# Performance work log

Measured on AMD Instinct MI355X. Metric: run time of the kernel, lower is better.

## Reference

```python
import jax, jax.numpy as jnp
import numpy as np

EPS = 1e-6

def setup_inputs() -> dict:
    key = jax.random.key(0)
    ks = jax.random.split(key, 8)
    I, S, O = 1024, 512, 1024
    Bsz, T = 4, 2048
    return {
        "u": jax.random.normal(ks[0], (Bsz, T, I), dtype=jnp.float32),
        "dt": jax.random.normal(ks[1], (S,), dtype=jnp.float32),
        "A": jax.random.normal(ks[2], (S,), dtype=jnp.float32),
        "Bmat": jax.random.normal(ks[3], (I, S), dtype=jnp.float32) / np.sqrt(S),
        "C": jax.random.normal(ks[4], (S, O), dtype=jnp.float32) / np.sqrt(S),
        "D": jax.random.normal(ks[5], (O,), dtype=jnp.float32),
        "norm_w": jnp.ones((I,), dtype=jnp.float32),
    }

def _rmsnorm(x, w):
    x32 = x.astype(jnp.float32)
    n = x32 * jax.lax.rsqrt(jnp.mean(x32 * x32, axis=-1, keepdims=True) + EPS)
    return n.astype(x.dtype) * w

def reference(u, dt, A, Bmat, C, D, norm_w):
    u = _rmsnorm(u, norm_w)                      # [B, T, I]
    Bsz, T, _ = u.shape
    dts = jax.nn.sigmoid(dt)                     # [S]
    a = jnp.exp(-dts * jnp.abs(A))               # [S] discretized decay
    t = jnp.arange(T, dtype=jnp.float32)
    h = dts[:, None] * a[:, None] ** t[None, :]  # [S, T] geometric kernel
    u_proj = jnp.einsum('bti,is->bst', u, Bmat)  # [B, S, T]
    # depthwise causal conv: flipped kernel + cross-correlation == convolution
    k = jnp.flip(h, axis=1)[:, None, :]          # [S, 1, T] (OIW)
    x = jax.lax.conv_general_dilated(
        u_proj, k, window_strides=(1,), padding=[(T - 1, T - 1)],
        dimension_numbers=('NCW', 'OIW', 'NCW'),
        feature_group_count=u_proj.shape[1])[:, :, :T]  # [B, S, T]
    x = jnp.transpose(x, (0, 2, 1))              # [B, T, S]
    y = jnp.einsum('bts,so->bto', x, C) + D      # [B, T, O]
    return (y, x[:, -1])
```

## Files before the change

kernel.cpp:

```cpp
#include <hip/hip_runtime.h>
#include <math.h>

#define I_DIM 1024
#define S_DIM 512
#define O_DIM 1024
#define T_DIM 2048
#define B_SZ 4
#define M_ROWS (B_SZ * T_DIM)
#define EPSF 1e-6f

#define CL 64
#define NCH 32

typedef _Float16 f16;
typedef __attribute__((ext_vector_type(8))) _Float16 f16x8;
typedef __attribute__((ext_vector_type(2))) _Float16 f16x2;
typedef __attribute__((ext_vector_type(4))) float f32x4;

__device__ __forceinline__ unsigned short f2h_bits(float f) {
    _Float16 h = (_Float16)f;
    return __builtin_bit_cast(unsigned short, h);
}

__device__ __forceinline__ void load16_lds(const void* g, void* l) {
    __builtin_amdgcn_global_load_lds((const __attribute__((address_space(1))) void*)g,
                                     (__attribute__((address_space(3))) void*)l,
                                     16, 0, 0);
}

__global__ __launch_bounds__(256)
void prep_w(const float* __restrict__ Bmat, const float* __restrict__ dt,
            const float* __restrict__ nw, unsigned short* __restrict__ Bt16,
            const float* __restrict__ Cmat, unsigned short* __restrict__ Ct16) {
    __shared__ float tile[32][33];
    const int t = threadIdx.x;
    const int tx = t & 31, ty = t >> 5;
    const int bx = blockIdx.x;
    if (bx < 512) {
        const int bs = (bx & 15) * 32;
        const int bi = (bx >> 4) * 32;
        #pragma unroll
        for (int i = ty; i < 32; i += 8)
            tile[i][tx] = Bmat[(size_t)(bi + i) * S_DIM + bs + tx];
        __syncthreads();
        const float w = nw[bi + tx];
        #pragma unroll
        for (int i = ty; i < 32; i += 8) {
            const int s = bs + i;
            const float dts = 1.0f / (1.0f + expf(-dt[s]));
            Bt16[(size_t)s * I_DIM + bi + tx] = f2h_bits(tile[tx][i] * dts * w);
        }
    } else {
        const int tb = bx - 512;
        const int bo = (tb & 31) * 32;
        const int bs = (tb >> 5) * 32;
        #pragma unroll
        for (int i = ty; i < 32; i += 8)
            tile[i][tx] = Cmat[(size_t)(bs + i) * O_DIM + bo + tx];
        __syncthreads();
        #pragma unroll
        for (int i = ty; i < 32; i += 8)
            Ct16[(size_t)(bo + i) * S_DIM + bs + tx] = f2h_bits(tile[tx][i]);
    }
}

__global__ __launch_bounds__(256)
void gemm1_rms_chfin(const float* __restrict__ U, const f16* __restrict__ Bt,
                     f16* __restrict__ up, float* __restrict__ chlast,
                     const float* __restrict__ dt, const float* __restrict__ Avec) {
    constexpr int K = I_DIM, N = S_DIM, LDA = 80, NK = K / 32;
    __shared__ __align__(16) unsigned char AsB[2][64 * LDA];
    __shared__ f16 Bs[2][128 * 32];
    __shared__ float rsbuf[64];
    const int t = threadIdx.x;

    int bid = blockIdx.x;
    bid = (bid & 7) * 64 + (bid >> 3);
    const int n0 = (bid & 3) * 128;
    const int m0 = (bid >> 2) * 64;
    const int wid = t >> 6, lane = t & 63;
    const int wn = wid * 32, lr = lane & 15, kg = lane >> 4;

    const float* aptr = U + (size_t)(m0 + (t >> 2)) * K + (t & 3) * 8;
    const f16*  bptr = Bt + (size_t)(n0 + (t >> 2)) * K + (t & 3) * 8;
    unsigned char* adst0 = &AsB[0][(t >> 2) * LDA + (t & 3) * 16];
    unsigned char* adst1 = &AsB[1][(t >> 2) * LDA + (t & 3) * 16];

    float ss = 0.f;
    f32x4 acc[4][2];
    #pragma unroll
    for (int i = 0; i < 4; ++i)
        #pragma unroll
        for (int j = 0; j < 2; ++j) acc[i][j] = (f32x4){0.f, 0.f, 0.f, 0.f};

    float4 ra, rb;
    auto cvt_write = [&](unsigned char* dst) {
        ss += ra.x * ra.x + ra.y * ra.y + ra.z * ra.z + ra.w * ra.w
            + rb.x * rb.x + rb.y * rb.y + rb.z * rb.z + rb.w * rb.w;
        f16x8 h = { (_Float16)ra.x, (_Float16)ra.y, (_Float16)ra.z, (_Float16)ra.w,
                    (_Float16)rb.x, (_Float16)rb.y, (_Float16)rb.z, (_Float16)rb.w };
        *(f16x8*)dst = h;
    };

    load16_lds(bptr, &Bs[0][t * 8]);
    load16_lds(bptr + (size_t)64 * K, &Bs[0][2048 + t * 8]);
    ra = *(const float4*)(aptr);
    rb = *(const float4*)(aptr + 4);
    cvt_write(adst0);
    __syncthreads();

    for (int kt = 0; kt < NK; ++kt) {
        const int cur = kt & 1;
        if (kt + 1 < NK) {
            const int k1 = (kt + 1) * 32;
            load16_lds(bptr + k1, &Bs[cur ^ 1][t * 8]);
            load16_lds(bptr + (size_t)64 * K + k1, &Bs[cur ^ 1][2048 + t * 8]);
            ra = *(const float4*)(aptr + k1);
            rb = *(const float4*)(aptr + k1 + 4);
        }
        f16x8 af[4], bf[2];
        #pragma unroll
        for (int m = 0; m < 4; ++m)
            af[m] = *(const f16x8*)&AsB[cur][(m * 16 + lr) * LDA + kg * 16];
        #pragma unroll
        for (int n = 0; n < 2; ++n)
            bf[n] = *(const f16x8*)&Bs[cur][(wn + n * 16 + lr) * 32 + kg * 8];
        #pragma unroll
        for (int m = 0; m < 4; ++m)
            #pragma unroll
            for (int n = 0; n < 2; ++n)
                acc[m][n] = __builtin_amdgcn_mfma_f32_16x16x32_f16(af[m], bf[n], acc[m][n], 0, 0, 0);
        if (kt + 1 < NK) cvt_write(cur == 0 ? adst1 : adst0);
        __syncthreads();
    }

    ss += __shfl_xor(ss, 1, 64);
    ss += __shfl_xor(ss, 2, 64);
    if ((t & 3) == 0) rsbuf[t >> 2] = rsqrtf(ss * (1.0f / K) + EPSF);
    __syncthreads();

    const int cb = m0 >> 11;
    const int cc = (m0 >> 6) & (NCH - 1);
    #pragma unroll
    for (int n = 0; n < 2; ++n) {
        const int col = n0 + wn + n * 16 + lr;
        const float dts = 1.0f / (1.0f + expf(-dt[col]));
        const float e = dts * fabsf(Avec[col]);
        const float ainv = expf(e);
        float partial = 0.f;
        #pragma unroll
        for (int m = 0; m < 4; ++m) {
            const int row = m * 16 + kg * 4;
            f32x4 rs4 = *(const f32x4*)&rsbuf[row];
            float wgt = expf(-e * (float)(63 - row));
            #pragma unroll
            for (int j = 0; j < 4; ++j) {
                const float val = rs4[j] * acc[m][n][j];
                up[(size_t)(m0 + row + j) * N + col] = (_Float16)val;
                partial = fmaf(wgt, val, partial);
                wgt *= ainv;
            }
        }
        partial += __shfl_xor(partial, 16, 64);
        partial += __shfl_xor(partial, 32, 64);
        if (kg == 0)
            chlast[(size_t)(cb * NCH + cc) * S_DIM + col] = partial;
    }
}

__global__ __launch_bounds__(256)
void gemm2_scan(const f16* __restrict__ upb, const float* __restrict__ chlast,
                const f16* __restrict__ Ct, const float* __restrict__ Dvec,
                const float* __restrict__ dt, const float* __restrict__ Avec,
                float* __restrict__ y, float* __restrict__ xlast) {
    constexpr int K = S_DIM, N = O_DIM, NK = K / 32;
    __shared__ __align__(16) unsigned char As[64 * 1024];
    __shared__ f16 Bs[2][128 * 32];
    const int t = threadIdx.x;

    int bid = blockIdx.x;
    bid = (bid & 7) * 128 + (bid >> 3);
    const int n0 = (bid & 7) * 128;
    const int m0 = (bid >> 3) * 64;
    const int wid = t >> 6, lane = t & 63;
    const int wn = wid * 32, lr = lane & 15, kg = lane >> 4;

    const f16* bptr = Ct + (size_t)(n0 + (t >> 2)) * K + (t & 3) * 8;
    load16_lds(bptr, &Bs[0][t * 8]);
    load16_lds(bptr + (size_t)64 * K, &Bs[0][2048 + t * 8]);

    const int cc = (m0 >> 6) & (NCH - 1);
    const int cb = m0 >> 11;
    const int s0 = 2 * t;
    const float dts0 = 1.0f / (1.0f + expf(-dt[s0]));
    const float dts1 = 1.0f / (1.0f + expf(-dt[s0 + 1]));
    const float ab0 = fabsf(Avec[s0]), ab1 = fabsf(Avec[s0 + 1]);
    const float g0 = expf(-dts0 * ab0);
    const float g1 = expf(-dts1 * ab1);
    const float gCL0 = expf(-dts0 * ab0 * (float)CL);
    const float gCL1 = expf(-dts1 * ab1 * (float)CL);
    const float2* ch = (const float2*)chlast;
    float cy0 = 0.f, cy1 = 0.f;
    for (int j = 0; j < cc; ++j) {
        float2 f = ch[(size_t)(cb * NCH + j) * 256 + t];
        cy0 = fmaf(gCL0, cy0, f.x);
        cy1 = fmaf(gCL1, cy1, f.y);
    }

    const unsigned* up32 = (const unsigned*)upb;
    const size_t ub = (size_t)m0 * 256 + t;
    unsigned v[CL];
    #pragma unroll
    for (int j = 0; j < CL; ++j) v[j] = up32[ub + (size_t)j * 256];
    float x0 = cy0, x1 = cy1;
    #pragma unroll
    for (int j = 0; j < CL; ++j) {
        f16x2 h = __builtin_bit_cast(f16x2, v[j]);
        x0 = fmaf(g0, x0, (float)h.x);
        x1 = fmaf(g1, x1, (float)h.y);
        f16x2 o; o.x = (_Float16)x0; o.y = (_Float16)x1;
        v[j] = __builtin_bit_cast(unsigned, o);
    }
    #pragma unroll
    for (int j = 0; j < CL; ++j)
        *(unsigned*)&As[j * 1024 + ((t * 4) ^ ((j & 7) << 4))] = v[j];
    if (cc == NCH - 1)
        ((float2*)xlast)[cb * 256 + t] = make_float2(x0, x1);
    __syncthreads();

    f32x4 acc[4][2];
    #pragma unroll
    for (int i = 0; i < 4; ++i)
        #pragma unroll
        for (int j = 0; j < 2; ++j) acc[i][j] = (f32x4){0.f, 0.f, 0.f, 0.f};

    const int swz = (lr & 7) << 4;
    for (int kt = 0; kt < NK; ++kt) {
        const int cur = kt & 1;
        if (kt + 1 < NK) {
            const int k1 = (kt + 1) * 32;
            load16_lds(bptr + k1, &Bs[cur ^ 1][t * 8]);
            load16_lds(bptr + (size_t)64 * K + k1, &Bs[cur ^ 1][2048 + t * 8]);
        }
        f16x8 af[4], bf[2];
        #pragma unroll
        for (int m = 0; m < 4; ++m)
            af[m] = *(const f16x8*)&As[(m * 16 + lr) * 1024 + ((kt * 64 + kg * 16) ^ swz)];
        #pragma unroll
        for (int n = 0; n < 2; ++n)
            bf[n] = *(const f16x8*)&Bs[cur][(wn + n * 16 + lr) * 32 + kg * 8];
        #pragma unroll
        for (int m = 0; m < 4; ++m)
            #pragma unroll
            for (int n = 0; n < 2; ++n)
                acc[m][n] = __builtin_amdgcn_mfma_f32_16x16x32_f16(af[m], bf[n], acc[m][n], 0, 0, 0);
        __syncthreads();
    }

    #pragma unroll
    for (int n = 0; n < 2; ++n) {
        const int col = n0 + wn + n * 16 + lr;
        const float dv = Dvec[col];
        #pragma unroll
        for (int m = 0; m < 4; ++m) {
            const int row = m0 + m * 16 + kg * 4;
            #pragma unroll
            for (int j = 0; j < 4; ++j)
                y[(size_t)(row + j) * N + col] = acc[m][n][j] + dv;
        }
    }
}

extern "C" void kernel_launch(void* const* d_in, const int* in_sizes, int n_in,
                              void* d_out, int out_size, void* d_ws, size_t ws_size,
                              hipStream_t stream) {
    const float* u    = (const float*)d_in[0];
    const float* dt   = (const float*)d_in[1];
    const float* Avec = (const float*)d_in[2];
    const float* Bmat = (const float*)d_in[3];
    const float* Cmat = (const float*)d_in[4];
    const float* Dvec = (const float*)d_in[5];
    const float* nw   = (const float*)d_in[6];

    float* y     = (float*)d_out;
    float* xlast = y + (size_t)M_ROWS * O_DIM;

    char* w = (char*)d_ws;
    f16*            up16   = (f16*)(w);
    unsigned short* Bt16   = (unsigned short*)(w + 8388608);
    unsigned short* Ct16   = (unsigned short*)(w + 9437184);
    float*          chlast = (float*)(w + 10485760);

    prep_w<<<1024, 256, 0, stream>>>(Bmat, dt, nw, Bt16, Cmat, Ct16);

    gemm1_rms_chfin<<<512, 256, 0, stream>>>(u, (const f16*)Bt16, up16, chlast, dt, Avec);

    gemm2_scan<<<1024, 256, 0, stream>>>(up16, chlast, (const f16*)Ct16, Dvec,
                                         dt, Avec, y, xlast);
}
```

Measured before the change: 64.44 us.

## Swizzle B tiles in LDS and use explicit waitcnt barriers in both GEMMs

Applies an XOR swizzle to the B-tile columns when loading them into LDS and when reading them back, to reduce LDS bank conflicts on the B fragment reads. Replaces __syncthreads with hand-placed s_waitcnt vmcnt counts, s_barrier and sched_barrier, so the next tile's global-to-LDS loads can stay in flight while the current tile is computed. In gemm1 the fp32 A loads are moved ahead of the B loads so that vmcnt(4) waits only for the older loads. Hand-counted waitcnt values risk races if the compiler emits a different number of memory ops than assumed.

```diff
diff --git a/kernel.cpp b/kernel.cpp
--- a/kernel.cpp
+++ b/kernel.cpp
@@ -82,9 +82,11 @@
     const int wn = wid * 32, lr = lane & 15, kg = lane >> 4;
 
     const float* aptr = U + (size_t)(m0 + (t >> 2)) * K + (t & 3) * 8;
-    const f16*  bptr = Bt + (size_t)(n0 + (t >> 2)) * K + (t & 3) * 8;
+    const int bswz = ((t & 3) ^ ((t >> 3) & 3)) * 8;
+    const f16* bptr = Bt + (size_t)(n0 + (t >> 2)) * K + bswz;
     unsigned char* adst0 = &AsB[0][(t >> 2) * LDA + (t & 3) * 16];
     unsigned char* adst1 = &AsB[1][(t >> 2) * LDA + (t & 3) * 16];
+    const int bread = (kg ^ ((lr >> 1) & 3)) * 8;
 
     float ss = 0.f;
     f32x4 acc[4][2];
@@ -107,31 +109,42 @@
     ra = *(const float4*)(aptr);
     rb = *(const float4*)(aptr + 4);
     cvt_write(adst0);
-    __syncthreads();
+    asm volatile("s_waitcnt vmcnt(0) lgkmcnt(0)");
+    __builtin_amdgcn_s_barrier();
 
     for (int kt = 0; kt < NK; ++kt) {
         const int cur = kt & 1;
         if (kt + 1 < NK) {
             const int k1 = (kt + 1) * 32;
+            ra = *(const float4*)(aptr + k1);
+            rb = *(const float4*)(aptr + k1 + 4);
             load16_lds(bptr + k1, &Bs[cur ^ 1][t * 8]);
             load16_lds(bptr + (size_t)64 * K + k1, &Bs[cur ^ 1][2048 + t * 8]);
-            ra = *(const float4*)(aptr + k1);
-            rb = *(const float4*)(aptr + k1 + 4);
-        }
+            asm volatile("s_waitcnt vmcnt(4)");
+        } else {
+            asm volatile("s_waitcnt vmcnt(0)");
+        }
+        __builtin_amdgcn_s_barrier();
+        __builtin_amdgcn_sched_barrier(0);
+
         f16x8 af[4], bf[2];
         #pragma unroll
         for (int m = 0; m < 4; ++m)
             af[m] = *(const f16x8*)&AsB[cur][(m * 16 + lr) * LDA + kg * 16];
         #pragma unroll
         for (int n = 0; n < 2; ++n)
-            bf[n] = *(const f16x8*)&Bs[cur][(wn + n * 16 + lr) * 32 + kg * 8];
+            bf[n] = *(const f16x8*)&Bs[cur][(wn + n * 16 + lr) * 32 + bread];
         #pragma unroll
         for (int m = 0; m < 4; ++m)
             #pragma unroll
             for (int n = 0; n < 2; ++n)
                 acc[m][n] = __builtin_amdgcn_mfma_f32_16x16x32_f16(af[m], bf[n], acc[m][n], 0, 0, 0);
-        if (kt + 1 < NK) cvt_write(cur == 0 ? adst1 : adst0);
-        __syncthreads();
+
+        if (kt + 1 < NK)
+            cvt_write(cur == 0 ? adst1 : adst0);
+        asm volatile("s_waitcnt lgkmcnt(0)");
+        __builtin_amdgcn_sched_barrier(0);
+        __builtin_amdgcn_s_barrier();
     }
 
     ss += __shfl_xor(ss, 1, 64);
@@ -185,9 +198,11 @@
     const int wid = t >> 6, lane = t & 63;
     const int wn = wid * 32, lr = lane & 15, kg = lane >> 4;
 
-    const f16* bptr = Ct + (size_t)(n0 + (t >> 2)) * K + (t & 3) * 8;
+    const int bswz = ((t & 3) ^ ((t >> 3) & 3)) * 8;
+    const f16* bptr = Ct + (size_t)(n0 + (t >> 2)) * K + bswz;
     load16_lds(bptr, &Bs[0][t * 8]);
     load16_lds(bptr + (size_t)64 * K, &Bs[0][2048 + t * 8]);
+    const int bread = (kg ^ ((lr >> 1) & 3)) * 8;
 
     const int cc = (m0 >> 6) & (NCH - 1);
     const int cb = m0 >> 11;
@@ -241,20 +256,26 @@
             const int k1 = (kt + 1) * 32;
             load16_lds(bptr + k1, &Bs[cur ^ 1][t * 8]);
             load16_lds(bptr + (size_t)64 * K + k1, &Bs[cur ^ 1][2048 + t * 8]);
-        }
+            asm volatile("s_waitcnt vmcnt(2)");
+        } else {
+            asm volatile("s_waitcnt vmcnt(0)");
+        }
+        __builtin_amdgcn_s_barrier();
+        __builtin_amdgcn_sched_barrier(0);
+
         f16x8 af[4], bf[2];
         #pragma unroll
         for (int m = 0; m < 4; ++m)
             af[m] = *(const f16x8*)&As[(m * 16 + lr) * 1024 + ((kt * 64 + kg * 16) ^ swz)];
         #pragma unroll
         for (int n = 0; n < 2; ++n)
-            bf[n] = *(const f16x8*)&Bs[cur][(wn + n * 16 + lr) * 32 + kg * 8];
+            bf[n] = *(const f16x8*)&Bs[cur][(wn + n * 16 + lr) * 32 + bread];
         #pragma unroll
         for (int m = 0; m < 4; ++m)
             #pragma unroll
             for (int n = 0; n < 2; ++n)
                 acc[m][n] = __builtin_amdgcn_mfma_f32_16x16x32_f16(af[m], bf[n], acc[m][n], 0, 0, 0);
-        __syncthreads();
+        __builtin_amdgcn_s_barrier();
     }
 
     #pragma unroll
```

Result: slower. 66.48 us (+3.2%).

## Move RMSNorm to prep pass and triple-buffer gemm1 with async LDS loads

Applied to the files above, without the earlier changes.

RMSNorm and the fp16 conversion of u move into a separate prep pass that writes a normalized fp16 copy of u. gemm1 can then stream both operands straight into LDS with async global_load_lds, using a three-stage buffer and an XOR swizzle to reduce bank conflicts. gemm2 gets the same swizzle, explicit vmcnt waits with raw barriers, and a 4-way unrolled carry scan. The cost is an extra 16 MB fp16 write and re-read of u plus one more pass over the input.

```diff
diff --git a/kernel.cpp b/kernel.cpp
--- a/kernel.cpp
+++ b/kernel.cpp
@@ -29,16 +29,38 @@
 }
 
 __global__ __launch_bounds__(256)
-void prep_w(const float* __restrict__ Bmat, const float* __restrict__ dt,
-            const float* __restrict__ nw, unsigned short* __restrict__ Bt16,
-            const float* __restrict__ Cmat, unsigned short* __restrict__ Ct16) {
+void prep(const float* __restrict__ u, const float* __restrict__ nw,
+          unsigned short* __restrict__ u16,
+          const float* __restrict__ Bmat, const float* __restrict__ dt,
+          unsigned short* __restrict__ Bt16,
+          const float* __restrict__ Cmat, unsigned short* __restrict__ Ct16) {
     __shared__ float tile[32][33];
     const int t = threadIdx.x;
-    const int tx = t & 31, ty = t >> 5;
     const int bx = blockIdx.x;
-    if (bx < 512) {
-        const int bs = (bx & 15) * 32;
-        const int bi = (bx >> 4) * 32;
+
+    if (bx < M_ROWS) {
+        float4 v = ((const float4*)(u + (size_t)bx * I_DIM))[t];
+        float ss = v.x * v.x + v.y * v.y + v.z * v.z + v.w * v.w;
+        #pragma unroll
+        for (int off = 32; off > 0; off >>= 1) ss += __shfl_down(ss, off, 64);
+        if ((t & 63) == 0) tile[0][t >> 6] = ss;
+        __syncthreads();
+        if (t == 0)
+            tile[0][0] = rsqrtf((tile[0][0] + tile[0][1] + tile[0][2] + tile[0][3])
+                                * (1.0f / I_DIM) + EPSF);
+        __syncthreads();
+        const float rs = tile[0][0];
+        ushort4 o;
+        o.x = f2h_bits(v.x * rs);
+        o.y = f2h_bits(v.y * rs);
+        o.z = f2h_bits(v.z * rs);
+        o.w = f2h_bits(v.w * rs);
+        ((ushort4*)(u16 + (size_t)bx * I_DIM))[t] = o;
+    } else if (bx < M_ROWS + 512) {
+        const int tb = bx - M_ROWS;
+        const int bs = (tb & 15) * 32;
+        const int bi = (tb >> 4) * 32;
+        const int tx = t & 31, ty = t >> 5;
         #pragma unroll
         for (int i = ty; i < 32; i += 8)
             tile[i][tx] = Bmat[(size_t)(bi + i) * S_DIM + bs + tx];
@@ -51,9 +73,10 @@
             Bt16[(size_t)s * I_DIM + bi + tx] = f2h_bits(tile[tx][i] * dts * w);
         }
     } else {
-        const int tb = bx - 512;
+        const int tb = bx - M_ROWS - 512;
         const int bo = (tb & 31) * 32;
         const int bs = (tb >> 5) * 32;
+        const int tx = t & 31, ty = t >> 5;
         #pragma unroll
         for (int i = ty; i < 32; i += 8)
             tile[i][tx] = Cmat[(size_t)(bs + i) * O_DIM + bo + tx];
@@ -65,13 +88,12 @@
 }
 
 __global__ __launch_bounds__(256)
-void gemm1_rms_chfin(const float* __restrict__ U, const f16* __restrict__ Bt,
-                     f16* __restrict__ up, float* __restrict__ chlast,
-                     const float* __restrict__ dt, const float* __restrict__ Avec) {
-    constexpr int K = I_DIM, N = S_DIM, LDA = 80, NK = K / 32;
-    __shared__ __align__(16) unsigned char AsB[2][64 * LDA];
-    __shared__ f16 Bs[2][128 * 32];
-    __shared__ float rsbuf[64];
+void gemm1_chfin(const f16* __restrict__ A, const f16* __restrict__ Bt,
+                 f16* __restrict__ up, float* __restrict__ chlast,
+                 const float* __restrict__ dt, const float* __restrict__ Avec) {
+    constexpr int K = I_DIM, N = S_DIM, NK = K / 32;
+    __shared__ f16 As[3][64 * 32];
+    __shared__ f16 Bs[3][128 * 32];
     const int t = threadIdx.x;
 
     int bid = blockIdx.x;
@@ -81,63 +103,50 @@
     const int wid = t >> 6, lane = t & 63;
     const int wn = wid * 32, lr = lane & 15, kg = lane >> 4;
 
-    const float* aptr = U + (size_t)(m0 + (t >> 2)) * K + (t & 3) * 8;
-    const f16*  bptr = Bt + (size_t)(n0 + (t >> 2)) * K + (t & 3) * 8;
-    unsigned char* adst0 = &AsB[0][(t >> 2) * LDA + (t & 3) * 16];
-    unsigned char* adst1 = &AsB[1][(t >> 2) * LDA + (t & 3) * 16];
-
-    float ss = 0.f;
+    const int srcswz = ((t & 3) ^ ((t >> 3) & 3)) * 8;
+    const f16* aptr = A + (size_t)(m0 + (t >> 2)) * K + srcswz;
+    const f16* bptr = Bt + (size_t)(n0 + (t >> 2)) * K + srcswz;
+    const int rchunk = (kg ^ ((lr >> 1) & 3)) * 8;
+
     f32x4 acc[4][2];
     #pragma unroll
     for (int i = 0; i < 4; ++i)
         #pragma unroll
         for (int j = 0; j < 2; ++j) acc[i][j] = (f32x4){0.f, 0.f, 0.f, 0.f};
 
-    float4 ra, rb;
-    auto cvt_write = [&](unsigned char* dst) {
-        ss += ra.x * ra.x + ra.y * ra.y + ra.z * ra.z + ra.w * ra.w
-            + rb.x * rb.x + rb.y * rb.y + rb.z * rb.z + rb.w * rb.w;
-        f16x8 h = { (_Float16)ra.x, (_Float16)ra.y, (_Float16)ra.z, (_Float16)ra.w,
-                    (_Float16)rb.x, (_Float16)rb.y, (_Float16)rb.z, (_Float16)rb.w };
-        *(f16x8*)dst = h;
+    auto stage = [&](int kt, int buf) {
+        const int k0 = kt * 32;
+        load16_lds(aptr + k0, &As[buf][t * 8]);
+        load16_lds(bptr + k0, &Bs[buf][t * 8]);
+        load16_lds(bptr + (size_t)64 * K + k0, &Bs[buf][2048 + t * 8]);
     };
 
-    load16_lds(bptr, &Bs[0][t * 8]);
-    load16_lds(bptr + (size_t)64 * K, &Bs[0][2048 + t * 8]);
-    ra = *(const float4*)(aptr);
-    rb = *(const float4*)(aptr + 4);
-    cvt_write(adst0);
-    __syncthreads();
-
+    stage(0, 0);
+    stage(1, 1);
+    int bcur = 0, bst = 2;
     for (int kt = 0; kt < NK; ++kt) {
-        const int cur = kt & 1;
-        if (kt + 1 < NK) {
-            const int k1 = (kt + 1) * 32;
-            load16_lds(bptr + k1, &Bs[cur ^ 1][t * 8]);
-            load16_lds(bptr + (size_t)64 * K + k1, &Bs[cur ^ 1][2048 + t * 8]);
-            ra = *(const float4*)(aptr + k1);
-            rb = *(const float4*)(aptr + k1 + 4);
-        }
+        if (kt + 1 < NK) asm volatile("s_waitcnt vmcnt(3)");
+        else             asm volatile("s_waitcnt vmcnt(0)");
+        __builtin_amdgcn_s_barrier();
+        __builtin_amdgcn_sched_barrier(0);
+        if (kt + 2 < NK) stage(kt + 2, bst);
+
         f16x8 af[4], bf[2];
         #pragma unroll
         for (int m = 0; m < 4; ++m)
-            af[m] = *(const f16x8*)&AsB[cur][(m * 16 + lr) * LDA + kg * 16];
+            af[m] = *(const f16x8*)&As[bcur][(m * 16 + lr) * 32 + rchunk];
         #pragma unroll
         for (int n = 0; n < 2; ++n)
-            bf[n] = *(const f16x8*)&Bs[cur][(wn + n * 16 + lr) * 32 + kg * 8];
+            bf[n] = *(const f16x8*)&Bs[bcur][(wn + n * 16 + lr) * 32 + rchunk];
         #pragma unroll
         for (int m = 0; m < 4; ++m)
             #pragma unroll
             for (int n = 0; n < 2; ++n)
                 acc[m][n] = __builtin_amdgcn_mfma_f32_16x16x32_f16(af[m], bf[n], acc[m][n], 0, 0, 0);
-        if (kt + 1 < NK) cvt_write(cur == 0 ? adst1 : adst0);
-        __syncthreads();
-    }
-
-    ss += __shfl_xor(ss, 1, 64);
-    ss += __shfl_xor(ss, 2, 64);
-    if ((t & 3) == 0) rsbuf[t >> 2] = rsqrtf(ss * (1.0f / K) + EPSF);
-    __syncthreads();
+
+        bcur = (bcur == 2) ? 0 : bcur + 1;
+        bst  = (bst  == 2) ? 0 : bst  + 1;
+    }
 
     const int cb = m0 >> 11;
     const int cc = (m0 >> 6) & (NCH - 1);
@@ -151,11 +160,10 @@
         #pragma unroll
         for (int m = 0; m < 4; ++m) {
             const int row = m * 16 + kg * 4;
-            f32x4 rs4 = *(const f32x4*)&rsbuf[row];
             float wgt = expf(-e * (float)(63 - row));
             #pragma unroll
             for (int j = 0; j < 4; ++j) {
-                const float val = rs4[j] * acc[m][n][j];
+                const float val = acc[m][n][j];
                 up[(size_t)(m0 + row + j) * N + col] = (_Float16)val;
                 partial = fmaf(wgt, val, partial);
                 wgt *= ainv;
@@ -185,9 +193,11 @@
     const int wid = t >> 6, lane = t & 63;
     const int wn = wid * 32, lr = lane & 15, kg = lane >> 4;
 
-    const f16* bptr = Ct + (size_t)(n0 + (t >> 2)) * K + (t & 3) * 8;
+    const int srcswz = ((t & 3) ^ ((t >> 3) & 3)) * 8;
+    const f16* bptr = Ct + (size_t)(n0 + (t >> 2)) * K + srcswz;
     load16_lds(bptr, &Bs[0][t * 8]);
     load16_lds(bptr + (size_t)64 * K, &Bs[0][2048 + t * 8]);
+    const int rchunk = (kg ^ ((lr >> 1) & 3)) * 8;
 
     const int cc = (m0 >> 6) & (NCH - 1);
     const int cb = m0 >> 11;
@@ -201,10 +211,23 @@
     const float gCL1 = expf(-dts1 * ab1 * (float)CL);
     const float2* ch = (const float2*)chlast;
     float cy0 = 0.f, cy1 = 0.f;
-    for (int j = 0; j < cc; ++j) {
-        float2 f = ch[(size_t)(cb * NCH + j) * 256 + t];
-        cy0 = fmaf(gCL0, cy0, f.x);
-        cy1 = fmaf(gCL1, cy1, f.y);
+    {
+        int j = 0;
+        for (; j + 4 <= cc; j += 4) {
+            float2 f0 = ch[(size_t)(cb * NCH + j + 0) * 256 + t];
+            float2 f1 = ch[(size_t)(cb * NCH + j + 1) * 256 + t];
+            float2 f2 = ch[(size_t)(cb * NCH + j + 2) * 256 + t];
+            float2 f3 = ch[(size_t)(cb * NCH + j + 3) * 256 + t];
+            cy0 = fmaf(gCL0, cy0, f0.x); cy1 = fmaf(gCL1, cy1, f0.y);
+            cy0 = fmaf(gCL0, cy0, f1.x); cy1 = fmaf(gCL1, cy1, f1.y);
+            cy0 = fmaf(gCL0, cy0, f2.x); cy1 = fmaf(gCL1, cy1, f2.y);
+            cy0 = fmaf(gCL0, cy0, f3.x); cy1 = fmaf(gCL1, cy1, f3.y);
+        }
+        for (; j < cc; ++j) {
+            float2 f = ch[(size_t)(cb * NCH + j) * 256 + t];
+            cy0 = fmaf(gCL0, cy0, f.x);
+            cy1 = fmaf(gCL1, cy1, f.y);
+        }
     }
 
     const unsigned* up32 = (const unsigned*)upb;
@@ -241,20 +264,26 @@
             const int k1 = (kt + 1) * 32;
             load16_lds(bptr + k1, &Bs[cur ^ 1][t * 8]);
             load16_lds(bptr + (size_t)64 * K + k1, &Bs[cur ^ 1][2048 + t * 8]);
-        }
+            asm volatile("s_waitcnt vmcnt(2)");
+        } else {
+            asm volatile("s_waitcnt vmcnt(0)");
+        }
+        __builtin_amdgcn_s_barrier();
+        __builtin_amdgcn_sched_barrier(0);
+
         f16x8 af[4], bf[2];
         #pragma unroll
         for (int m = 0; m < 4; ++m)
             af[m] = *(const f16x8*)&As[(m * 16 + lr) * 1024 + ((kt * 64 + kg * 16) ^ swz)];
         #pragma unroll
         for (int n = 0; n < 2; ++n)
-            bf[n] = *(const f16x8*)&Bs[cur][(wn + n * 16 + lr) * 32 + kg * 8];
+            bf[n] = *(const f16x8*)&Bs[cur][(wn + n * 16 + lr) * 32 + rchunk];
         #pragma unroll
         for (int m = 0; m < 4; ++m)
             #pragma unroll
             for (int n = 0; n < 2; ++n)
                 acc[m][n] = __builtin_amdgcn_mfma_f32_16x16x32_f16(af[m], bf[n], acc[m][n], 0, 0, 0);
-        __syncthreads();
+        __builtin_amdgcn_s_barrier();
     }
 
     #pragma unroll
@@ -286,14 +315,16 @@
     float* xlast = y + (size_t)M_ROWS * O_DIM;
 
     char* w = (char*)d_ws;
-    f16*            up16   = (f16*)(w);
-    unsigned short* Bt16   = (unsigned short*)(w + 8388608);
-    unsigned short* Ct16   = (unsigned short*)(w + 9437184);
-    float*          chlast = (float*)(w + 10485760);
-
-    prep_w<<<1024, 256, 0, stream>>>(Bmat, dt, nw, Bt16, Cmat, Ct16);
-
-    gemm1_rms_chfin<<<512, 256, 0, stream>>>(u, (const f16*)Bt16, up16, chlast, dt, Avec);
+    unsigned short* u16    = (unsigned short*)(w);
+    f16*            up16   = (f16*)(w + 16777216);
+    unsigned short* Bt16   = (unsigned short*)(w + 25165824);
+    unsigned short* Ct16   = (unsigned short*)(w + 26214400);
+    float*          chlast = (float*)(w + 27262976);
+
+    prep<<<M_ROWS + 512 + 512, 256, 0, stream>>>(u, nw, u16, Bmat, dt, Bt16, Cmat, Ct16);
+
+    gemm1_chfin<<<512, 256, 0, stream>>>((const f16*)u16, (const f16*)Bt16,
+                                         up16, chlast, dt, Avec);
 
     gemm2_scan<<<1024, 256, 0, stream>>>(up16, chlast, (const f16*)Ct16, Dvec,
                                          dt, Avec, y, xlast);
```

Result: faster. 59.77 us (-7.2%).
